# Performance work log

Measured on AMD Instinct MI355X. Metric: run time of the kernel, lower is better.

The kernel has to match this reference:

```python
import jax, jax.numpy as jnp
import numpy as np

F = 256   # num_features
H = 64    # hidden_dim
DEPTH = 5 # -> 3 hidden-to-hidden layers
B = 16384


def setup_inputs() -> dict:
    key = jax.random.key(0)
    ks = jax.random.split(key, 7)
    x = jax.random.normal(ks[0], (B, F), dtype=jnp.float32)
    # per-feature params, batched over F (torch default init ~ U(-1/sqrt(fan_in), 1/sqrt(fan_in)))
    W1 = jax.random.uniform(ks[1], (F, H), jnp.float32, -1.0, 1.0)          # fan_in = 1
    b1 = jax.random.uniform(ks[2], (F, H), jnp.float32, -1.0, 1.0)
    lim = 1.0 / np.sqrt(H)
    Wh = jax.random.uniform(ks[3], (DEPTH - 2, F, H, H), jnp.float32, -lim, lim)
    bh = jax.random.uniform(ks[4], (DEPTH - 2, F, H), jnp.float32, -lim, lim)
    Wo = jax.random.uniform(ks[5], (F, H), jnp.float32, -lim, lim)
    bo = jax.random.uniform(ks[6], (F,), jnp.float32, -lim, lim)
    return {"x": x, "W1": W1, "b1": b1, "Wh": Wh, "bh": bh, "Wo": Wo, "bo": bo}


def reference(x, W1, b1, Wh, bh, Wo, bo):
    # first layer: scalar input per feature -> hidden. h: [B, F, H]
    h = x[:, :, None] * W1[None, :, :] + b1[None, :, :]
    # (depth-2) hidden layers: ReLU then per-feature GEMM (dropout p=0 -> no-op)
    for l in range(Wh.shape[0]):
        h = jnp.einsum('bfh,fhk->bfk', jax.nn.relu(h), Wh[l]) + bh[l][None]
    # output layer: hidden -> scalar per feature, then sum over features
    feats = jnp.einsum('bfh,fh->bf', jax.nn.relu(h), Wo) + bo[None, :]
    return feats.sum(axis=1)  # [B]
```

## Files before the change

kernel.cpp:

```cpp
#include <hip/hip_runtime.h>

typedef _Float16 f16;
typedef f16    f16x2 __attribute__((ext_vector_type(2)));
typedef f16    f16x4 __attribute__((ext_vector_type(4)));
typedef f16    f16x8 __attribute__((ext_vector_type(8)));
typedef __fp16 fp16x2 __attribute__((ext_vector_type(2)));
typedef float  f32x4 __attribute__((ext_vector_type(4)));

#define NF 256
#define NH 64
#define NL 3
#define NB 3
#define NWAVE 4
#define MT (NB * 16 * NWAVE)
#define NTHR (NWAVE * 64)
#define WFRAG (NH * NH)

union U2  { f16x8 v8; f16x2 h[4]; };
union WB1 { f16x8 v8; fp16x2 p[4]; };
union WO4 { f16x4 v4; fp16x2 p[2]; };


__device__ __forceinline__ f16x2 pkmax(float a, float b) {
    fp16x2 p = __builtin_amdgcn_cvt_pkrtz(a, b);
    fp16x2 z = {(__fp16)0.f, (__fp16)0.f};
    p = __builtin_elementwise_max(p, z);
    return __builtin_bit_cast(f16x2, p);
}
__device__ __forceinline__ f16x2 pkfmarelu(fp16x2 x, fp16x2 w, fp16x2 b) {
    fp16x2 p = __builtin_elementwise_fma(x, w, b);
    fp16x2 z = {(__fp16)0.f, (__fp16)0.f};
    p = __builtin_elementwise_max(p, z);
    return __builtin_bit_cast(f16x2, p);
}
__device__ __forceinline__ float dot2(f16x2 a, fp16x2 b, float c) {
#if __has_builtin(__builtin_amdgcn_fdot2)
    return __builtin_amdgcn_fdot2(__builtin_bit_cast(fp16x2, a), b, c, false);
#else
    return fmaf((float)a[0], (float)b[0], fmaf((float)a[1], (float)b[1], c));
#endif
}

__global__ __launch_bounds__(256) void presplit_w(
    const float* __restrict__ Wh, f16* __restrict__ wsWh)
{
    __shared__ float wld[NH * NH];
    const int lf = blockIdx.x;
    const int t  = threadIdx.x;
    const float* __restrict__ src = Wh + (size_t)lf * WFRAG;
#pragma unroll
    for (int i = 0; i < 4; ++i)
        *(f32x4*)&wld[(i * 256 + t) * 4] = *(const f32x4*)&src[(i * 256 + t) * 4];
    __syncthreads();
#pragma unroll
    for (int g2 = 0; g2 < 2; ++g2) {
        const int g  = g2 * 256 + t;
        const int ln = g & 63, ks = (g >> 6) & 1, mt = g >> 7;
        const int cl = ln & 15, gr = ln >> 4;
        const int m  = mt * 16 + cl;
        f16x8 hi;
#pragma unroll
        for (int jj = 0; jj < 8; ++jj) {
            const int u = 32 * ks + 16 * (jj >> 2) + 4 * gr + (jj & 3);
            hi[jj] = (f16)wld[u * NH + m];
        }
        *(f16x8*)&wsWh[((size_t)lf * 512 + g) * 8] = hi;
    }
}

__global__ __launch_bounds__(64) void prepack_small(
    const float* __restrict__ W1, const float* __restrict__ b1,
    const float* __restrict__ Wo,
    f16* __restrict__ wsW1B, f16* __restrict__ wsWo)
{
    const int f = blockIdx.x;
    const int t = threadIdx.x;
    if (t < 16) {
        const int gr = t & 3, jq = (t >> 2) & 1, ks = t >> 3;
        const int ub = 32 * ks + 16 * jq + 4 * gr;
        f16x8 o;
#pragma unroll
        for (int i = 0; i < 4; ++i) o[i]     = (f16)W1[f * NH + ub + i];
#pragma unroll
        for (int i = 0; i < 4; ++i) o[4 + i] = (f16)b1[f * NH + ub + i];
        *(f16x8*)&wsW1B[((size_t)f * 16 + t) * 8] = o;
    } else if (t < 32) {
        const int s = t - 16;
        const int mt = s >> 2, gr = s & 3;
        f16x4 o;
#pragma unroll
        for (int i = 0; i < 4; ++i)
            o[i] = (f16)Wo[f * NH + mt * 16 + gr * 4 + i];
        *(f16x4*)&wsWo[((size_t)f * 16 + s) * 4] = o;
    }
}

template <bool PRE>
__global__ __launch_bounds__(NTHR, 5) void permlp_v14(
    const float* __restrict__ x,
    const float* __restrict__ W1,
    const float* __restrict__ b1,
    const float* __restrict__ Wh,
    const float* __restrict__ bh,
    const float* __restrict__ Wo,
    const float* __restrict__ bo,
    const f16* __restrict__ wsWh,
    const f16* __restrict__ wsW1B,
    const f16* __restrict__ wsWo,
    float* __restrict__ out,
    int nby, int Btot)
{
    const int nwg  = NF * nby;
    const int q    = nwg >> 3;
    const int bid  = blockIdx.x;
    const int wgid = (bid & 7) * q + (bid >> 3);
    const int f    = wgid / nby;
    const int by   = wgid - f * nby;

    const int tid = threadIdx.x;
    const int wv  = tid >> 6;
    const int ln  = tid & 63;
    const int cl  = ln & 15;
    const int gr  = ln >> 4;
    const int gb0 = by * MT + wv * (NB * 16);

    auto loadW = [&](const f16* __restrict__ baseH, const float* __restrict__ Wl,
                     int mt, f16x8 (&A)[2]) {
#pragma unroll
        for (int ks = 0; ks < 2; ++ks) {
            if constexpr (PRE) {
                A[ks] = *(const f16x8*)&baseH[(size_t)((mt * 2 + ks) * 64 + ln) * 8];
            } else {
                const int m = mt * 16 + cl;
                f16x8 hi8;
#pragma unroll
                for (int j = 0; j < 8; ++j) {
                    const int u = 32 * ks + 16 * (j >> 2) + 4 * gr + (j & 3);
                    hi8[j] = (f16)Wl[(size_t)u * NH + m];
                }
                A[ks] = hi8;
            }
        }
    };

    U2 HA[NB][2], HB[NB][2];
    {
        fp16x2 xx[NB];
#pragma unroll
        for (int bt = 0; bt < NB; ++bt) {
            const int row = gb0 + bt * 16 + cl;
            const float xv = (row < Btot) ? x[(size_t)row * NF + f] : 0.f;
            xx[bt] = __builtin_amdgcn_cvt_pkrtz(xv, xv);
        }
        if constexpr (PRE) {
            const f16* __restrict__ wb1 = wsW1B + (size_t)f * 128;
#pragma unroll
            for (int ks = 0; ks < 2; ++ks)
#pragma unroll
                for (int jq = 0; jq < 2; ++jq) {
                    WB1 wb;
                    wb.v8 = *(const f16x8*)&wb1[(size_t)((ks * 2 + jq) * 4 + gr) * 8];
#pragma unroll
                    for (int bt = 0; bt < NB; ++bt) {
                        HA[bt][ks].h[jq * 2]     = pkfmarelu(xx[bt], wb.p[0], wb.p[2]);
                        HA[bt][ks].h[jq * 2 + 1] = pkfmarelu(xx[bt], wb.p[1], wb.p[3]);
                    }
                }
        } else {
            const float* __restrict__ w1 = W1 + f * NH;
            const float* __restrict__ bb = b1 + f * NH;
#pragma unroll
            for (int ks = 0; ks < 2; ++ks)
#pragma unroll
                for (int jq = 0; jq < 2; ++jq) {
                    const int ub = 32 * ks + 16 * jq + 4 * gr;
                    const f32x4 w4 = *(const f32x4*)&w1[ub];
                    const f32x4 b4 = *(const f32x4*)&bb[ub];
#pragma unroll
                    for (int bt = 0; bt < NB; ++bt) {
                        float xv = (float)xx[bt][0];
                        HA[bt][ks].h[jq * 2]     = pkmax(fmaf(xv, w4[0], b4[0]), fmaf(xv, w4[1], b4[1]));
                        HA[bt][ks].h[jq * 2 + 1] = pkmax(fmaf(xv, w4[2], b4[2]), fmaf(xv, w4[3], b4[3]));
                    }
                }
        }
    }

    auto hidden = [&](U2 (&I)[NB][2], U2 (&O)[NB][2], const int l) {
        const f16* __restrict__ baseH = PRE ? wsWh + (size_t)(l * NF + f) * 4096 : nullptr;
        const float* __restrict__ Wl  = Wh + (size_t)(l * NF + f) * WFRAG;
        const float* __restrict__ bl  = bh + (size_t)(l * NF + f) * NH;
#pragma unroll
        for (int mt = 0; mt < 4; ++mt) {
            f16x8 WA[2];
            loadW(baseH, Wl, mt, WA);
            const f32x4 bias4 = *(const f32x4*)&bl[mt * 16 + gr * 4];
            f32x4 acc[NB];
#pragma unroll
            for (int bt = 0; bt < NB; ++bt) acc[bt] = bias4;
#pragma unroll
            for (int ks = 0; ks < 2; ++ks)
#pragma unroll
                for (int bt = 0; bt < NB; ++bt)
                    acc[bt] = __builtin_amdgcn_mfma_f32_16x16x32_f16(WA[ks], I[bt][ks].v8, acc[bt], 0, 0, 0);
#pragma unroll
            for (int bt = 0; bt < NB; ++bt) {
                O[bt][mt >> 1].h[(mt & 1) * 2]     = pkmax(acc[bt][0], acc[bt][1]);
                O[bt][mt >> 1].h[(mt & 1) * 2 + 1] = pkmax(acc[bt][2], acc[bt][3]);
            }
        }
    };

    hidden(HA, HB, 0);
    hidden(HB, HA, 1);

    float souts[NB];
#pragma unroll
    for (int bt = 0; bt < NB; ++bt) souts[bt] = 0.f;
    {
        const int l = NL - 1;
        const f16* __restrict__ baseH = PRE ? wsWh + (size_t)(l * NF + f) * 4096 : nullptr;
        const float* __restrict__ Wl  = Wh + (size_t)(l * NF + f) * WFRAG;
        const float* __restrict__ bl  = bh + (size_t)(l * NF + f) * NH;
#pragma unroll
        for (int mt = 0; mt < 4; ++mt) {
            f16x8 WA[2];
            loadW(baseH, Wl, mt, WA);
            const f32x4 bias4 = *(const f32x4*)&bl[mt * 16 + gr * 4];
            f32x4 acc[NB];
#pragma unroll
            for (int bt = 0; bt < NB; ++bt) acc[bt] = bias4;
#pragma unroll
            for (int ks = 0; ks < 2; ++ks)
#pragma unroll
                for (int bt = 0; bt < NB; ++bt)
                    acc[bt] = __builtin_amdgcn_mfma_f32_16x16x32_f16(WA[ks], HA[bt][ks].v8, acc[bt], 0, 0, 0);
            if constexpr (PRE) {
                WO4 wo;
                wo.v4 = *(const f16x4*)&wsWo[((size_t)f * 16 + mt * 4 + gr) * 4];
#pragma unroll
                for (int bt = 0; bt < NB; ++bt) {
                    f16x2 p01 = pkmax(acc[bt][0], acc[bt][1]);
                    f16x2 p23 = pkmax(acc[bt][2], acc[bt][3]);
                    souts[bt] = dot2(p01, wo.p[0], souts[bt]);
                    souts[bt] = dot2(p23, wo.p[1], souts[bt]);
                }
            } else {
                const f32x4 wov4 = *(const f32x4*)&Wo[f * NH + mt * 16 + gr * 4];
#pragma unroll
                for (int bt = 0; bt < NB; ++bt)
#pragma unroll
                    for (int i = 0; i < 4; ++i)
                        souts[bt] = fmaf(fmaxf(acc[bt][i], 0.f), wov4[i], souts[bt]);
            }
        }
    }

    const float bof = bo[f];
#pragma unroll
    for (int bt = 0; bt < NB; ++bt) {
        float s = souts[bt];
        s += __shfl_xor(s, 16, 64);
        s += __shfl_xor(s, 32, 64);
        const int row = gb0 + bt * 16 + ln;
        if (ln < 16 && row < Btot)
            atomicAdd(&out[row], s + bof);
    }
}

extern "C" void kernel_launch(void* const* d_in, const int* in_sizes, int n_in,
                              void* d_out, int out_size, void* d_ws, size_t ws_size,
                              hipStream_t stream)
{
    const float* x  = (const float*)d_in[0];
    const float* W1 = (const float*)d_in[1];
    const float* b1 = (const float*)d_in[2];
    const float* Wh = (const float*)d_in[3];
    const float* bh = (const float*)d_in[4];
    const float* Wo = (const float*)d_in[5];
    const float* bo = (const float*)d_in[6];
    float* out = (float*)d_out;

    const int B   = in_sizes[0] / NF;
    const int nby = (B + MT - 1) / MT;

    hipMemsetAsync(out, 0, (size_t)out_size * sizeof(float), stream);

    const size_t whElems  = (size_t)NL * NF * WFRAG;
    const size_t w1bElems = (size_t)NF * 16 * 8;
    const size_t woElems  = (size_t)NF * 16 * 4;
    const size_t needW    = (whElems + w1bElems + woElems) * sizeof(f16);
    dim3 grid(NF * nby);

    if (ws_size >= needW) {
        f16* wsWh  = (f16*)d_ws;
        f16* wsW1B = wsWh + whElems;
        f16* wsWo  = wsW1B + w1bElems;
        presplit_w<<<NL * NF, 256, 0, stream>>>(Wh, wsWh);
        prepack_small<<<NF, 64, 0, stream>>>(W1, b1, Wo, wsW1B, wsWo);
        permlp_v14<true><<<grid, dim3(NTHR), 0, stream>>>(
            x, W1, b1, Wh, bh, Wo, bo, wsWh, wsW1B, wsWo, out, nby, B);
    } else {
        permlp_v14<false><<<grid, dim3(NTHR), 0, stream>>>(
            x, W1, b1, Wh, bh, Wo, bo, nullptr, nullptr, nullptr, out, nby, B);
    }
}
```

Before: 162.3 us.

## Raise batch tiles per wave to four and double-buffer hidden weight fragments

Increases batch sub-tiles per wave from 3 to 4, so each weight fragment load feeds more MFMAs, and lowers the occupancy hint to 4. Prefetches the next mt's weight fragments while computing the current one to hide load latency. Removes the batch-boundary checks and uses floor division for the tile count, which assumes the batch is a multiple of 256. Higher register use may reduce occupancy.

```diff
diff --git a/kernel.cpp b/kernel.cpp
--- a/kernel.cpp
+++ b/kernel.cpp
@@ -10,7 +10,7 @@
 #define NF 256
 #define NH 64
 #define NL 3
-#define NB 3
+#define NB 4
 #define NWAVE 4
 #define MT (NB * 16 * NWAVE)
 #define NTHR (NWAVE * 64)
@@ -96,7 +96,7 @@
 }
 
 template <bool PRE>
-__global__ __launch_bounds__(NTHR, 5) void permlp_v14(
+__global__ __launch_bounds__(NTHR, 4) void permlp_v15(
     const float* __restrict__ x,
     const float* __restrict__ W1,
     const float* __restrict__ b1,
@@ -108,7 +108,7 @@
     const f16* __restrict__ wsW1B,
     const f16* __restrict__ wsWo,
     float* __restrict__ out,
-    int nby, int Btot)
+    int nby)
 {
     const int nwg  = NF * nby;
     const int q    = nwg >> 3;
@@ -148,8 +148,7 @@
         fp16x2 xx[NB];
 #pragma unroll
         for (int bt = 0; bt < NB; ++bt) {
-            const int row = gb0 + bt * 16 + cl;
-            const float xv = (row < Btot) ? x[(size_t)row * NF + f] : 0.f;
+            const float xv = x[(size_t)(gb0 + bt * 16 + cl) * NF + f];
             xx[bt] = __builtin_amdgcn_cvt_pkrtz(xv, xv);
         }
         if constexpr (PRE) {
@@ -178,7 +177,7 @@
                     const f32x4 b4 = *(const f32x4*)&bb[ub];
 #pragma unroll
                     for (int bt = 0; bt < NB; ++bt) {
-                        float xv = (float)xx[bt][0];
+                        const float xv = (float)xx[bt][0];
                         HA[bt][ks].h[jq * 2]     = pkmax(fmaf(xv, w4[0], b4[0]), fmaf(xv, w4[1], b4[1]));
                         HA[bt][ks].h[jq * 2 + 1] = pkmax(fmaf(xv, w4[2], b4[2]), fmaf(xv, w4[3], b4[3]));
                     }
@@ -190,10 +189,12 @@
         const f16* __restrict__ baseH = PRE ? wsWh + (size_t)(l * NF + f) * 4096 : nullptr;
         const float* __restrict__ Wl  = Wh + (size_t)(l * NF + f) * WFRAG;
         const float* __restrict__ bl  = bh + (size_t)(l * NF + f) * NH;
+        f16x8 WA[2][2];
+        loadW(baseH, Wl, 0, WA[0]);
 #pragma unroll
         for (int mt = 0; mt < 4; ++mt) {
-            f16x8 WA[2];
-            loadW(baseH, Wl, mt, WA);
+            if (mt < 3)
+                loadW(baseH, Wl, mt + 1, WA[(mt + 1) & 1]);
             const f32x4 bias4 = *(const f32x4*)&bl[mt * 16 + gr * 4];
             f32x4 acc[NB];
 #pragma unroll
@@ -202,7 +203,7 @@
             for (int ks = 0; ks < 2; ++ks)
 #pragma unroll
                 for (int bt = 0; bt < NB; ++bt)
-                    acc[bt] = __builtin_amdgcn_mfma_f32_16x16x32_f16(WA[ks], I[bt][ks].v8, acc[bt], 0, 0, 0);
+                    acc[bt] = __builtin_amdgcn_mfma_f32_16x16x32_f16(WA[mt & 1][ks], I[bt][ks].v8, acc[bt], 0, 0, 0);
 #pragma unroll
             for (int bt = 0; bt < NB; ++bt) {
                 O[bt][mt >> 1].h[(mt & 1) * 2]     = pkmax(acc[bt][0], acc[bt][1]);
@@ -222,10 +223,12 @@
         const f16* __restrict__ baseH = PRE ? wsWh + (size_t)(l * NF + f) * 4096 : nullptr;
         const float* __restrict__ Wl  = Wh + (size_t)(l * NF + f) * WFRAG;
         const float* __restrict__ bl  = bh + (size_t)(l * NF + f) * NH;
+        f16x8 WA[2][2];
+        loadW(baseH, Wl, 0, WA[0]);
 #pragma unroll
         for (int mt = 0; mt < 4; ++mt) {
-            f16x8 WA[2];
-            loadW(baseH, Wl, mt, WA);
+            if (mt < 3)
+                loadW(baseH, Wl, mt + 1, WA[(mt + 1) & 1]);
             const f32x4 bias4 = *(const f32x4*)&bl[mt * 16 + gr * 4];
             f32x4 acc[NB];
 #pragma unroll
@@ -234,7 +237,7 @@
             for (int ks = 0; ks < 2; ++ks)
 #pragma unroll
                 for (int bt = 0; bt < NB; ++bt)
-                    acc[bt] = __builtin_amdgcn_mfma_f32_16x16x32_f16(WA[ks], HA[bt][ks].v8, acc[bt], 0, 0, 0);
+                    acc[bt] = __builtin_amdgcn_mfma_f32_16x16x32_f16(WA[mt & 1][ks], HA[bt][ks].v8, acc[bt], 0, 0, 0);
             if constexpr (PRE) {
                 WO4 wo;
                 wo.v4 = *(const f16x4*)&wsWo[((size_t)f * 16 + mt * 4 + gr) * 4];
@@ -262,9 +265,8 @@
         float s = souts[bt];
         s += __shfl_xor(s, 16, 64);
         s += __shfl_xor(s, 32, 64);
-        const int row = gb0 + bt * 16 + ln;
-        if (ln < 16 && row < Btot)
-            atomicAdd(&out[row], s + bof);
+        if (ln < 16)
+            atomicAdd(&out[gb0 + bt * 16 + ln], s + bof);
     }
 }
 
@@ -282,7 +284,7 @@
     float* out = (float*)d_out;
 
     const int B   = in_sizes[0] / NF;
-    const int nby = (B + MT - 1) / MT;
+    const int nby = B / MT;
 
     hipMemsetAsync(out, 0, (size_t)out_size * sizeof(float), stream);
 
@@ -298,10 +300,10 @@
         f16* wsWo  = wsW1B + w1bElems;
         presplit_w<<<NL * NF, 256, 0, stream>>>(Wh, wsWh);
         prepack_small<<<NF, 64, 0, stream>>>(W1, b1, Wo, wsW1B, wsWo);
-        permlp_v14<true><<<grid, dim3(NTHR), 0, stream>>>(
-            x, W1, b1, Wh, bh, Wo, bo, wsWh, wsW1B, wsWo, out, nby, B);
+        permlp_v15<true><<<grid, dim3(NTHR), 0, stream>>>(
+            x, W1, b1, Wh, bh, Wo, bo, wsWh, wsW1B, wsWo, out, nby);
     } else {
-        permlp_v14<false><<<grid, dim3(NTHR), 0, stream>>>(
-            x, W1, b1, Wh, bh, Wo, bo, nullptr, nullptr, nullptr, out, nby, B);
-    }
-}
+        permlp_v15<false><<<grid, dim3(NTHR), 0, stream>>>(
+            x, W1, b1, Wh, bh, Wo, bo, nullptr, nullptr, nullptr, out, nby);
+    }
+}
```

After: 133.6 us. 1.21x faster.
